# Performance work log

Measured on AMD Instinct MI355X. Metric: run time of the kernel, lower is better.

## Reference

```python
import jax, jax.numpy as jnp
import numpy as np

NUM_C = 1000
B, L = 8, 1024
D, H, NB, DFF = 512, 8, 4, 2048
DK = D // H
EPS = 1e-5


def _ln(x, s, b):
    mu = jnp.mean(x, axis=-1, keepdims=True)
    var = jnp.mean((x - mu) ** 2, axis=-1, keepdims=True)
    return (x - mu) * jax.lax.rsqrt(var + EPS) * s + b


def setup_inputs() -> dict:
    key = jax.random.key(0)
    ks = iter(jax.random.split(key, 64))

    def nrm(shape, scale=0.02):
        return jax.random.normal(next(ks), shape, dtype=jnp.float32) * scale

    inp = {
        "q": jax.random.randint(next(ks), (B, L), 0, NUM_C),
        "r": jax.random.randint(next(ks), (B, L), 0, 2),
        # embeddings
        "ctx_emb": nrm((NUM_C * 2, D)),
        "val_emb": nrm((NUM_C * 2, D)),
        "skill_emb": nrm((NUM_C, D)),
        "pos_emb": nrm((L, D)),
        # attention projections, stacked over blocks
        "Wq": nrm((NB, D, D)), "bq": jnp.zeros((NB, D)),
        "Wk": nrm((NB, D, D)), "bk": jnp.zeros((NB, D)),
        "Wv": nrm((NB, D, D)), "bv": jnp.zeros((NB, D)),
        "Wo": nrm((NB, D, D)), "bo": jnp.zeros((NB, D)),
        # layer norms (ctx / val streams, pre- and post-FFN)
        "ln1c_s": jnp.ones((NB, D)), "ln1c_b": jnp.zeros((NB, D)),
        "ln1v_s": jnp.ones((NB, D)), "ln1v_b": jnp.zeros((NB, D)),
        "ln2c_s": jnp.ones((NB, D)), "ln2c_b": jnp.zeros((NB, D)),
        "ln2v_s": jnp.ones((NB, D)), "ln2v_b": jnp.zeros((NB, D)),
        # FFNs
        "fc1c_W": nrm((NB, D, DFF)), "fc1c_b": jnp.zeros((NB, DFF)),
        "fc2c_W": nrm((NB, DFF, D)), "fc2c_b": jnp.zeros((NB, D)),
        "fc1v_W": nrm((NB, D, DFF)), "fc1v_b": jnp.zeros((NB, DFF)),
        "fc2v_W": nrm((NB, DFF, D)), "fc2v_b": jnp.zeros((NB, D)),
        # prediction head: [3D -> DFF -> 256 -> 1]
        "hW1": nrm((3 * D, DFF)), "hb1": jnp.zeros((DFF,)),
        "hW2": nrm((DFF, 256)), "hb2": jnp.zeros((256,)),
        "hW3": nrm((256, 1)), "hb3": jnp.zeros((1,)),
    }
    return inp


def reference(q, r, ctx_emb, val_emb, skill_emb, pos_emb,
              Wq, bq, Wk, bk, Wv, bv, Wo, bo,
              ln1c_s, ln1c_b, ln1v_s, ln1v_b,
              ln2c_s, ln2c_b, ln2v_s, ln2v_b,
              fc1c_W, fc1c_b, fc2c_W, fc2c_b,
              fc1v_W, fc1v_b, fc2v_W, fc2v_b,
              hW1, hb1, hW2, hb2, hW3, hb3):
    inter = q + NUM_C * r                       # [B, L] interaction ids
    pos = pos_emb[None, :L, :]
    ctx = ctx_emb[inter] + pos                  # [B, L, D]
    val = val_emb[inter] + pos                  # [B, L, D]
    causal = jnp.tril(jnp.ones((L, L), dtype=bool))
    scale = 1.0 / (DK ** 0.5)

    for i in range(NB):
        # dual-stream MHA: Q,K from ctx; V from val
        Q = (ctx @ Wq[i] + bq[i]).reshape(B, L, H, DK)
        K = (ctx @ Wk[i] + bk[i]).reshape(B, L, H, DK)
        V = (val @ Wv[i] + bv[i]).reshape(B, L, H, DK)
        # fp32 scores (as in torch source), mask==0 -> -inf, softmax
        scores = jnp.einsum('bqhd,bkhd->bhqk', Q.astype(jnp.float32),
                            K.astype(jnp.float32)) * scale
        scores = jnp.where(causal, scores, -jnp.inf)
        attn = jax.nn.softmax(scores, axis=-1)  # dropout = identity (eval)
        out = jnp.einsum('bhqk,bkhd->bqhd', attn, V).reshape(B, L, D)
        out = out @ Wo[i] + bo[i]
        # shared attn output added to both streams, separate norms
        ctx = _ln(ctx + out, ln1c_s[i], ln1c_b[i])
        val = _ln(val + out, ln1v_s[i], ln1v_b[i])
        # dual FFNs
        f_ctx = jax.nn.relu(ctx @ fc1c_W[i] + fc1c_b[i]) @ fc2c_W[i] + fc2c_b[i]
        ctx = _ln(ctx + f_ctx, ln2c_s[i], ln2c_b[i])
        f_val = jax.nn.relu(val @ fc1v_W[i] + fc1v_b[i]) @ fc2v_W[i] + fc2v_b[i]
        val = _ln(val + f_val, ln2v_s[i], ln2v_b[i])

    feat = jnp.concatenate([ctx, val, skill_emb[q]], axis=-1)  # [B, L, 3D]
    h = jax.nn.relu(feat @ hW1 + hb1)
    h = jax.nn.relu(h @ hW2 + hb2)
    logits = (h @ hW3 + hb3)[..., 0]
    return jax.nn.sigmoid(logits)               # [B, L] p(correct)
```

## Files before the change

kernel.cpp:

```cpp
#include <hip/hip_runtime.h>
#include <hip/hip_bf16.h>
#include <math.h>

#define TOK 8192
#define DM 512
#define NH 8
#define DKH 64
#define DFFN 2048
#define SEQ 1024
#define NBLK 4
#define NUMC 1000

typedef __attribute__((ext_vector_type(8))) short bf16x8;
typedef __attribute__((ext_vector_type(4))) float f32x4;
typedef __attribute__((ext_vector_type(4))) ushort u16x4;
typedef __hip_bfloat16 bf16;

__device__ __forceinline__ void gload_lds16(const ushort* g, ushort* l) {
    __builtin_amdgcn_global_load_lds(
        (const __attribute__((address_space(1))) void*)g,
        (__attribute__((address_space(3))) void*)l, 16, 0, 0);
}

__device__ __forceinline__ void wgbar() {
    asm volatile("" ::: "memory");
    __builtin_amdgcn_s_barrier();
    asm volatile("" ::: "memory");
}

__global__ __launch_bounds__(256) void embed_kernel(
    const int* __restrict__ q, const int* __restrict__ r,
    const float* __restrict__ ctx_emb, const float* __restrict__ val_emb,
    const float* __restrict__ pos_emb,
    float* __restrict__ ctx32, float* __restrict__ val32,
    bf16* __restrict__ ctx16, bf16* __restrict__ val16)
{
    const int t = blockIdx.x;
    const int inter = q[t] + NUMC * r[t];
    const int l = t & (SEQ - 1);
    const float* ce = ctx_emb + (size_t)inter * DM;
    const float* ve = val_emb + (size_t)inter * DM;
    const float* pe = pos_emb + (size_t)l * DM;
    const size_t o = (size_t)t * DM;
    for (int d = threadIdx.x; d < DM; d += 256) {
        float p = pe[d];
        float c = ce[d] + p;
        float v = ve[d] + p;
        ctx32[o + d] = c; val32[o + d] = v;
        ctx16[o + d] = __float2bfloat16(c);
        val16[o + d] = __float2bfloat16(v);
    }
}

__global__ __launch_bounds__(256) void transpose_kernel(
    const float* __restrict__ src, bf16* __restrict__ dst,
    int K, int N, long sb, long db)
{
    __shared__ float t[32][33];
    src += (long)blockIdx.z * sb;
    dst += (long)blockIdx.z * db;
    const int n0 = blockIdx.x * 32;
    const int k0 = blockIdx.y * 32;
    const int tx = threadIdx.x;
    const int ty = threadIdx.y;
    for (int i = ty; i < 32; i += 8) t[i][tx] = src[(size_t)(k0 + i) * N + n0 + tx];
    __syncthreads();
    for (int i = ty; i < 32; i += 8)
        dst[(size_t)(n0 + i) * K + k0 + tx] = __float2bfloat16(t[tx][i]);
}

template<int BN, bool OUTBF16>
__global__ __launch_bounds__(256, 3) void mfma_gemm(
    const ushort* __restrict__ A, const ushort* __restrict__ Bt,
    const float* __restrict__ bias1, const float* __restrict__ bias2, int split,
    void* __restrict__ Cv, int N, int K, int relu, int vtmode,
    const ushort* __restrict__ A1, const ushort* __restrict__ Bt1,
    const float* __restrict__ bias1_1, void* __restrict__ Cv1)
{
    if (blockIdx.z) { A = A1; Bt = Bt1; bias1 = bias1_1; Cv = Cv1; }
    constexpr int MI = (BN == 128) ? 4 : 2;
    constexpr int BR = BN / 32;
    __shared__ ushort As[128 * 64];
    __shared__ ushort Bs[BN * 64];
    const int tid = threadIdx.x;
    const int wave = tid >> 6;
    const int lane = tid & 63;
    const int ln = lane & 15;
    const int kq = lane >> 4;
    const int nx = gridDim.x;
    const int lin = blockIdx.x + nx * blockIdx.y;
    const int loc = lin >> 3;
    const int mdiv = loc / nx;
    const int bm = ((lin & 7) + 8 * mdiv) * 128;
    const int bn = (loc - mdiv * nx) * BN;
    const int wr = (BN == 128) ? (wave >> 1) * 64 : wave * 32;
    const int wc = (BN == 128) ? (wave & 1) * 64 : 0;

    const int trow = tid >> 3;
    const int gcb = (tid & 7) ^ (trow & 7);
    const ushort* Ab = A + (size_t)(bm + trow) * K + gcb * 8;
    const ushort* Bb = Bt + (size_t)(bn + trow) * K + gcb * 8;
    ushort* AsW = As + wave * 512;
    ushort* BsW = Bs + wave * 512;

    f32x4 acc[MI][4];
#pragma unroll
    for (int i = 0; i < MI; ++i)
#pragma unroll
        for (int j = 0; j < 4; ++j) acc[i][j] = (f32x4){0.f, 0.f, 0.f, 0.f};

    for (int k0 = 0; k0 < K; k0 += 64) {
        __syncthreads();
#pragma unroll
        for (int p = 0; p < 4; ++p)
            gload_lds16(Ab + (size_t)32 * p * K + k0, AsW + p * 2048);
#pragma unroll
        for (int p = 0; p < BR; ++p)
            gload_lds16(Bb + (size_t)32 * p * K + k0, BsW + p * 2048);
        __syncthreads();
#pragma unroll
        for (int half = 0; half < 2; ++half) {
            const int cb = ((half * 4 + kq) ^ (ln & 7)) * 8;
            bf16x8 bfr[4];
#pragma unroll
            for (int j = 0; j < 4; ++j)
                bfr[j] = *(const bf16x8*)&Bs[(wc + j * 16 + ln) * 64 + cb];
#pragma unroll
            for (int i = 0; i < MI; ++i) {
                const bf16x8 af = *(const bf16x8*)&As[(wr + i * 16 + ln) * 64 + cb];
#pragma unroll
                for (int j = 0; j < 4; ++j)
                    acc[i][j] = __builtin_amdgcn_mfma_f32_16x16x32_bf16(af, bfr[j], acc[i][j], 0, 0, 0);
            }
        }
    }

#pragma unroll
    for (int i = 0; i < MI; ++i) {
        const int rowb = bm + wr + i * 16 + kq * 4;
#pragma unroll
        for (int j = 0; j < 4; ++j) {
            const int colg = bn + wc + j * 16 + ln;
            const float bv = (colg < split) ? bias1[colg] : bias2[colg - split];
            if (vtmode) {
                union { u16x4 v; ushort u[4]; } pk;
#pragma unroll
                for (int rr = 0; rr < 4; ++rr) {
                    float v = acc[i][j][rr] + bv;
                    bf16 t = __float2bfloat16(v);
                    pk.u[rr] = *(ushort*)&t;
                }
                *(u16x4*)((ushort*)Cv + ((size_t)(rowb >> 10) * 512 + colg) * 1024 + (rowb & 1023)) = pk.v;
            } else {
#pragma unroll
                for (int rr = 0; rr < 4; ++rr) {
                    float v = acc[i][j][rr] + bv;
                    if (relu) v = fmaxf(v, 0.f);
                    if (OUTBF16)
                        ((bf16*)Cv)[(size_t)(rowb + rr) * N + colg] = __float2bfloat16(v);
                    else
                        ((float*)Cv)[(size_t)(rowb + rr) * N + colg] = v;
                }
            }
        }
    }
}

__device__ __forceinline__ void stage256(const ushort* Ag, const ushort* Bg,
                                         ushort* AsD, ushort* BsD, int K, int kk)
{
#pragma unroll
    for (int p = 0; p < 4; ++p)
        gload_lds16(Ag + (size_t)(64 * p) * K + kk, AsD + p * 4096);
#pragma unroll
    for (int p = 0; p < 4; ++p)
        gload_lds16(Bg + (size_t)(64 * p) * K + kk, BsD + p * 4096);
}

__global__ __launch_bounds__(512, 2) void mfma_gemm256(
    const ushort* __restrict__ A, const ushort* __restrict__ Bt,
    const float* __restrict__ bias, bf16* __restrict__ C, int N, int K, int relu,
    const ushort* __restrict__ A1, const ushort* __restrict__ Bt1,
    const float* __restrict__ bias1, bf16* __restrict__ C1)
{
    if (blockIdx.z) { A = A1; Bt = Bt1; bias = bias1; C = C1; }
    __shared__ ushort As[2 * 16384];
    __shared__ ushort Bs[2 * 16384];
    const int tid = threadIdx.x;
    const int wave = tid >> 6, lane = tid & 63;
    const int ln = lane & 15, kq = lane >> 4;
    const int wr = wave >> 2;
    const int wc = wave & 3;

    const int nx = gridDim.x;
    const int lin = blockIdx.x + nx * blockIdx.y;
    const int loc = lin >> 3;
    const int mdiv = loc / nx;
    const int bm = ((lin & 7) + 8 * mdiv) * 256;
    const int bn = (loc - mdiv * nx) * 256;

    const int srow = tid >> 3;
    const int sgcb = (tid & 7) ^ (srow & 7);
    const ushort* Ag = A + (size_t)(bm + srow) * K + sgcb * 8;
    const ushort* Bg = Bt + (size_t)(bn + srow) * K + sgcb * 8;
    const int wofs = wave * 512;

    f32x4 acc[8][4];
#pragma unroll
    for (int i = 0; i < 8; ++i)
#pragma unroll
        for (int j = 0; j < 4; ++j) acc[i][j] = (f32x4){0.f, 0.f, 0.f, 0.f};

    const int NT = K >> 6;
    stage256(Ag, Bg, As + wofs, Bs + wofs, K, 0);

    for (int t = 0; t < NT; ++t) {
        const int b = t & 1;
        const int k0 = t << 6;
        if (t + 1 < NT) {
            stage256(Ag, Bg, As + (b ^ 1) * 16384 + wofs, Bs + (b ^ 1) * 16384 + wofs, K, k0 + 64);
            asm volatile("s_waitcnt vmcnt(8)" ::: "memory");
        } else {
            asm volatile("s_waitcnt vmcnt(0)" ::: "memory");
        }
        wgbar();

        const ushort* Asb = As + b * 16384;
        const ushort* Bsb = Bs + b * 16384;
        bf16x8 bf[4][2];
#pragma unroll
        for (int j = 0; j < 4; ++j)
#pragma unroll
            for (int h = 0; h < 2; ++h)
                bf[j][h] = *(const bf16x8*)&Bsb[(wc * 64 + j * 16 + ln) * 64 + (((h * 4 + kq) ^ (ln & 7)) * 8)];
#pragma unroll
        for (int q = 0; q < 4; ++q) {
            bf16x8 af0[2], af1[2];
#pragma unroll
            for (int h = 0; h < 2; ++h) {
                af0[h] = *(const bf16x8*)&Asb[(wr * 128 + (2 * q) * 16 + ln) * 64 + (((h * 4 + kq) ^ (ln & 7)) * 8)];
                af1[h] = *(const bf16x8*)&Asb[(wr * 128 + (2 * q + 1) * 16 + ln) * 64 + (((h * 4 + kq) ^ (ln & 7)) * 8)];
            }
            __builtin_amdgcn_s_setprio(1);
#pragma unroll
            for (int h = 0; h < 2; ++h)
#pragma unroll
                for (int j = 0; j < 4; ++j) {
                    acc[2 * q][j]     = __builtin_amdgcn_mfma_f32_16x16x32_bf16(af0[h], bf[j][h], acc[2 * q][j], 0, 0, 0);
                    acc[2 * q + 1][j] = __builtin_amdgcn_mfma_f32_16x16x32_bf16(af1[h], bf[j][h], acc[2 * q + 1][j], 0, 0, 0);
                }
            __builtin_amdgcn_s_setprio(0);
            wgbar();
        }
    }

#pragma unroll
    for (int i = 0; i < 8; ++i) {
        const int gr = bm + wr * 128 + i * 16 + kq * 4;
#pragma unroll
        for (int j = 0; j < 4; ++j) {
            const int gc = bn + wc * 64 + j * 16 + ln;
            const float bv = bias[gc];
#pragma unroll
            for (int rr = 0; rr < 4; ++rr) {
                float v = acc[i][j][rr] + bv;
                if (relu) v = fmaxf(v, 0.f);
                C[(size_t)(gr + rr) * N + gc] = __float2bfloat16(v);
            }
        }
    }
}

__global__ __launch_bounds__(256) void attn_kernel(
    const bf16* __restrict__ QK, const bf16* __restrict__ Vt,
    bf16* __restrict__ Og)
{
    __shared__ ushort Qs[64 * 64];
    __shared__ ushort Ks[64 * 64];
    __shared__ ushort Vs[64 * 64];
    __shared__ ushort Ps[4 * 16 * 68];

    const int tid = threadIdx.x;
    const int wave = tid >> 6, lane = tid & 63;
    const int ln = lane & 15, kq = lane >> 4;
    const int lin = blockIdx.x + 16 * blockIdx.y;
    const int loc = lin >> 3;
    const int qt = loc & 15;
    const int bh = (lin & 7) + 8 * (loc >> 4);
    const int b = bh >> 3, h = bh & 7;

    const int srow = tid >> 3;
    const int sgcb = (tid & 7) ^ (srow & 7);
    const ushort* gQ = (const ushort*)QK + (size_t)(b * SEQ + qt * 64 + srow) * 1024 + h * 64 + sgcb * 8;
    const ushort* gK = (const ushort*)QK + (size_t)(b * SEQ + srow) * 1024 + 512 + h * 64 + sgcb * 8;
    const ushort* gV = (const ushort*)Vt + (size_t)(bh * 64 + srow) * 1024 + sgcb * 8;
    ushort* QsW = Qs + wave * 512;
    ushort* KsW = Ks + wave * 512;
    ushort* VsW = Vs + wave * 512;

    gload_lds16(gQ, QsW);
    gload_lds16(gQ + 32 * 1024, QsW + 2048);

    float rs[4];
    f32x4 oacc[4];
#pragma unroll
    for (int r = 0; r < 4; ++r) { rs[r] = 0.f; oacc[r] = (f32x4){0.f, 0.f, 0.f, 0.f}; }
    const float sc2 = 0.125f * 1.4426950408889634f;

    const int cb0 = (kq ^ (ln & 7)) * 8;
    const int cb1 = ((4 + kq) ^ (ln & 7)) * 8;

    for (int kt = 0; kt <= qt; ++kt) {
        __syncthreads();
        gload_lds16(gK + (size_t)kt * 64 * 1024, KsW);
        gload_lds16(gK + (size_t)(kt * 64 + 32) * 1024, KsW + 2048);
        gload_lds16(gV + kt * 64, VsW);
        gload_lds16(gV + 32 * 1024 + kt * 64, VsW + 2048);
        __syncthreads();

        const bf16x8 aq0 = *(const bf16x8*)&Qs[(wave * 16 + ln) * 64 + cb0];
        const bf16x8 aq1 = *(const bf16x8*)&Qs[(wave * 16 + ln) * 64 + cb1];
        f32x4 s[4];
#pragma unroll
        for (int c = 0; c < 4; ++c) {
            const bf16x8 bk0 = *(const bf16x8*)&Ks[(c * 16 + ln) * 64 + cb0];
            const bf16x8 bk1 = *(const bf16x8*)&Ks[(c * 16 + ln) * 64 + cb1];
            s[c] = (f32x4){0.f, 0.f, 0.f, 0.f};
            s[c] = __builtin_amdgcn_mfma_f32_16x16x32_bf16(aq0, bk0, s[c], 0, 0, 0);
            s[c] = __builtin_amdgcn_mfma_f32_16x16x32_bf16(aq1, bk1, s[c], 0, 0, 0);
        }
        if (kt == qt) {
#pragma unroll
            for (int c = 0; c < 4; ++c)
#pragma unroll
                for (int r = 0; r < 4; ++r) {
                    const int qg = wave * 16 + kq * 4 + r;
                    const int jg = c * 16 + ln;
                    const float pv = (jg <= qg) ? exp2f(s[c][r] * sc2) : 0.f;
                    rs[r] += pv;
                    *(bf16*)&Ps[wave * 1088 + (kq * 4 + r) * 68 + c * 16 + ln] = __float2bfloat16(pv);
                }
        } else {
#pragma unroll
            for (int c = 0; c < 4; ++c)
#pragma unroll
                for (int r = 0; r < 4; ++r) {
                    const float pv = exp2f(s[c][r] * sc2);
                    rs[r] += pv;
                    *(bf16*)&Ps[wave * 1088 + (kq * 4 + r) * 68 + c * 16 + ln] = __float2bfloat16(pv);
                }
        }
        const bf16x8 ap0 = *(const bf16x8*)&Ps[wave * 1088 + ln * 68 + kq * 8];
        const bf16x8 ap1 = *(const bf16x8*)&Ps[wave * 1088 + ln * 68 + 32 + kq * 8];
#pragma unroll
        for (int c2 = 0; c2 < 4; ++c2) {
            const bf16x8 bv0 = *(const bf16x8*)&Vs[(c2 * 16 + ln) * 64 + cb0];
            const bf16x8 bv1 = *(const bf16x8*)&Vs[(c2 * 16 + ln) * 64 + cb1];
            oacc[c2] = __builtin_amdgcn_mfma_f32_16x16x32_bf16(ap0, bv0, oacc[c2], 0, 0, 0);
            oacc[c2] = __builtin_amdgcn_mfma_f32_16x16x32_bf16(ap1, bv1, oacc[c2], 0, 0, 0);
        }
    }
    float inv[4];
#pragma unroll
    for (int r = 0; r < 4; ++r) {
        float v = rs[r];
        v += __shfl_xor(v, 1);
        v += __shfl_xor(v, 2);
        v += __shfl_xor(v, 4);
        v += __shfl_xor(v, 8);
        inv[r] = 1.f / v;
    }
#pragma unroll
    for (int c2 = 0; c2 < 4; ++c2)
#pragma unroll
        for (int r = 0; r < 4; ++r)
            Og[(size_t)(b * SEQ + qt * 64 + wave * 16 + kq * 4 + r) * 512 + h * 64 + c2 * 16 + ln]
                = __float2bfloat16(oacc[c2][r] * inv[r]);
}

__global__ __launch_bounds__(256) void lnp_kernel(
    const float* __restrict__ x0, const bf16* __restrict__ r0, const float* __restrict__ s0,
    const float* __restrict__ b0, float* __restrict__ of0, bf16* __restrict__ oh0,
    const float* __restrict__ x1, const bf16* __restrict__ r1, const float* __restrict__ s1,
    const float* __restrict__ b1, float* __restrict__ of1, bf16* __restrict__ oh1)
{
    const float* x = x0; const bf16* res = r0; const float* s = s0; const float* bb = b0;
    float* of = of0; bf16* oh = oh0;
    if (blockIdx.y) { x = x1; res = r1; s = s1; bb = b1; of = of1; oh = oh1; }
    __shared__ float w1[4], w2[4];
    const size_t o = (size_t)blockIdx.x * DM;
    const int i0 = threadIdx.x, i1 = threadIdx.x + 256;
    const float v0 = x[o + i0] + __bfloat162float(res[o + i0]);
    const float v1 = x[o + i1] + __bfloat162float(res[o + i1]);
    float sum = v0 + v1;
#pragma unroll
    for (int off = 32; off; off >>= 1) sum += __shfl_down(sum, off);
    if ((threadIdx.x & 63) == 0) w1[threadIdx.x >> 6] = sum;
    __syncthreads();
    const float mu = (w1[0] + w1[1] + w1[2] + w1[3]) * (1.f / DM);
    const float d0 = v0 - mu, d1 = v1 - mu;
    float vs = d0 * d0 + d1 * d1;
#pragma unroll
    for (int off = 32; off; off >>= 1) vs += __shfl_down(vs, off);
    if ((threadIdx.x & 63) == 0) w2[threadIdx.x >> 6] = vs;
    __syncthreads();
    const float rstd = rsqrtf((w2[0] + w2[1] + w2[2] + w2[3]) * (1.f / DM) + 1e-5f);
    const float o0 = d0 * rstd * s[i0] + bb[i0];
    const float o1 = d1 * rstd * s[i1] + bb[i1];
    of[o + i0] = o0; of[o + i1] = o1;
    oh[o + i0] = __float2bfloat16(o0);
    oh[o + i1] = __float2bfloat16(o1);
}

__global__ __launch_bounds__(256) void gather_kernel(
    const bf16* __restrict__ ctx16, const bf16* __restrict__ val16,
    const float* __restrict__ skill, const int* __restrict__ q,
    bf16* __restrict__ feat)
{
    const int t = blockIdx.x;
    const float* sp = skill + (size_t)q[t] * DM;
    const bf16* cp = ctx16 + (size_t)t * DM;
    const bf16* vp = val16 + (size_t)t * DM;
    bf16* fp = feat + (size_t)t * (3 * DM);
    for (int d = threadIdx.x; d < DM; d += 256) {
        fp[d] = cp[d];
        fp[DM + d] = vp[d];
        fp[2 * DM + d] = __float2bfloat16(sp[d]);
    }
}

__global__ __launch_bounds__(256) void logits_kernel(
    const float* __restrict__ h2, const float* __restrict__ w,
    const float* __restrict__ bptr, float* __restrict__ out)
{
    __shared__ float w1[4];
    const int t = blockIdx.x;
    float sum = h2[(size_t)t * 256 + threadIdx.x] * w[threadIdx.x];
#pragma unroll
    for (int off = 32; off; off >>= 1) sum += __shfl_down(sum, off);
    if ((threadIdx.x & 63) == 0) w1[threadIdx.x >> 6] = sum;
    __syncthreads();
    if (threadIdx.x == 0) {
        const float logit = w1[0] + w1[1] + w1[2] + w1[3] + bptr[0];
        out[t] = 1.f / (1.f + __expf(-logit));
    }
}

extern "C" void kernel_launch(void* const* d_in, const int* in_sizes, int n_in,
                              void* d_out, int out_size, void* d_ws, size_t ws_size,
                              hipStream_t stream)
{
    const int*   q         = (const int*)d_in[0];
    const int*   r         = (const int*)d_in[1];
    const float* ctx_emb   = (const float*)d_in[2];
    const float* val_emb   = (const float*)d_in[3];
    const float* skill_emb = (const float*)d_in[4];
    const float* pos_emb   = (const float*)d_in[5];
    const float* Wq = (const float*)d_in[6];
    const float* bq = (const float*)d_in[7];
    const float* Wk = (const float*)d_in[8];
    const float* bk = (const float*)d_in[9];
    const float* Wv = (const float*)d_in[10];
    const float* bv = (const float*)d_in[11];
    const float* Wo = (const float*)d_in[12];
    const float* bo = (const float*)d_in[13];
    const float* ln1c_s = (const float*)d_in[14];
    const float* ln1c_b = (const float*)d_in[15];
    const float* ln1v_s = (const float*)d_in[16];
    const float* ln1v_b = (const float*)d_in[17];
    const float* ln2c_s = (const float*)d_in[18];
    const float* ln2c_b = (const float*)d_in[19];
    const float* ln2v_s = (const float*)d_in[20];
    const float* ln2v_b = (const float*)d_in[21];
    const float* fc1c_W = (const float*)d_in[22];
    const float* fc1c_b = (const float*)d_in[23];
    const float* fc2c_W = (const float*)d_in[24];
    const float* fc2c_b = (const float*)d_in[25];
    const float* fc1v_W = (const float*)d_in[26];
    const float* fc1v_b = (const float*)d_in[27];
    const float* fc2v_W = (const float*)d_in[28];
    const float* fc2v_b = (const float*)d_in[29];
    const float* hW1 = (const float*)d_in[30];
    const float* hb1 = (const float*)d_in[31];
    const float* hW2 = (const float*)d_in[32];
    const float* hb2 = (const float*)d_in[33];
    const float* hW3 = (const float*)d_in[34];
    const float* hb3 = (const float*)d_in[35];
    float* out = (float*)d_out;

    char* p = (char*)d_ws;
    auto alloc = [&](size_t bytes) { char* ret = p; p += bytes; return ret; };
    float* ctx32 = (float*)alloc(16777216);
    float* val32 = (float*)alloc(16777216);
    bf16*  ob16c = (bf16*)alloc(8388608);
    bf16*  ob16v = (bf16*)alloc(8388608);
    bf16*  ctx16 = (bf16*)alloc(8388608);
    bf16*  val16 = (bf16*)alloc(8388608);
    bf16*  qk16  = (bf16*)alloc(16777216);
    bf16*  v16pad= (bf16*)alloc(8388608);
    bf16*  vt16  = (bf16*)alloc(8388608);
    bf16*  att16 = (bf16*)alloc(8388608);
    bf16*  mid16c = (bf16*)alloc(33554432);
    bf16*  qkT   = (bf16*)alloc(4194304);
    bf16*  vT    = (bf16*)alloc(2097152);
    bf16*  oT    = (bf16*)alloc(2097152);
    bf16*  fc1cT = (bf16*)alloc(8388608);
    bf16*  fc2cT = (bf16*)alloc(8388608);
    bf16*  fc1vT = (bf16*)alloc(8388608);
    bf16*  fc2vT = (bf16*)alloc(8388608);
    bf16*  hW1T  = (bf16*)alloc(6291456);
    bf16*  hW2T  = (bf16*)alloc(1048576);
    (void)v16pad;
    bf16*  mid16v = qk16;
    bf16*  feat16 = qk16;
    float* h2     = (float*)vt16;

    const dim3 tb(32, 8);
    transpose_kernel<<<dim3(16, 16, 4), tb, 0, stream>>>(Wq, qkT,          512, 512, 262144, 524288);
    transpose_kernel<<<dim3(16, 16, 4), tb, 0, stream>>>(Wk, qkT + 262144, 512, 512, 262144, 524288);
    transpose_kernel<<<dim3(16, 16, 4), tb, 0, stream>>>(Wv, vT, 512, 512, 262144, 262144);
    transpose_kernel<<<dim3(16, 16, 4), tb, 0, stream>>>(Wo, oT, 512, 512, 262144, 262144);
    transpose_kernel<<<dim3(64, 16, 4), tb, 0, stream>>>(fc1c_W, fc1cT, 512, 2048, 1048576, 1048576);
    transpose_kernel<<<dim3(16, 64, 4), tb, 0, stream>>>(fc2c_W, fc2cT, 2048, 512, 1048576, 1048576);
    transpose_kernel<<<dim3(64, 16, 4), tb, 0, stream>>>(fc1v_W, fc1vT, 512, 2048, 1048576, 1048576);
    transpose_kernel<<<dim3(16, 64, 4), tb, 0, stream>>>(fc2v_W, fc2vT, 2048, 512, 1048576, 1048576);
    transpose_kernel<<<dim3(64, 48, 1), tb, 0, stream>>>(hW1, hW1T, 1536, 2048, 0, 0);
    transpose_kernel<<<dim3(8, 64, 1),  tb, 0, stream>>>(hW2, hW2T, 2048, 256, 0, 0);

    embed_kernel<<<TOK, 256, 0, stream>>>(q, r, ctx_emb, val_emb, pos_emb,
                                          ctx32, val32, ctx16, val16);

    for (int i = 0; i < NBLK; ++i) {
        mfma_gemm<128, true><<<dim3(8, 64), 256, 0, stream>>>(
            (const ushort*)ctx16, (const ushort*)(qkT + (size_t)i * 524288),
            bq + i * DM, bk + i * DM, 512, qk16, 1024, 512, 0, 0,
            nullptr, nullptr, nullptr, nullptr);
        mfma_gemm<64, true><<<dim3(8, 64), 256, 0, stream>>>(
            (const ushort*)val16, (const ushort*)(vT + (size_t)i * 262144),
            bv + i * DM, nullptr, 1 << 30, vt16, 512, 512, 0, 1,
            nullptr, nullptr, nullptr, nullptr);
        attn_kernel<<<dim3(16, 64), 256, 0, stream>>>(qk16, vt16, att16);
        mfma_gemm<64, true><<<dim3(8, 64), 256, 0, stream>>>(
            (const ushort*)att16, (const ushort*)(oT + (size_t)i * 262144),
            bo + i * DM, nullptr, 1 << 30, ob16c, 512, 512, 0, 0,
            nullptr, nullptr, nullptr, nullptr);
        lnp_kernel<<<dim3(TOK, 2), 256, 0, stream>>>(
            ctx32, ob16c, ln1c_s + i * DM, ln1c_b + i * DM, ctx32, ctx16,
            val32, ob16c, ln1v_s + i * DM, ln1v_b + i * DM, val32, val16);
        mfma_gemm256<<<dim3(8, 32, 2), 512, 0, stream>>>(
            (const ushort*)ctx16, (const ushort*)(fc1cT + (size_t)i * 1048576),
            fc1c_b + i * DFFN, mid16c, 2048, 512, 1,
            (const ushort*)val16, (const ushort*)(fc1vT + (size_t)i * 1048576),
            fc1v_b + i * DFFN, mid16v);
        mfma_gemm<128, true><<<dim3(4, 64, 2), 256, 0, stream>>>(
            (const ushort*)mid16c, (const ushort*)(fc2cT + (size_t)i * 1048576),
            fc2c_b + i * DM, nullptr, 1 << 30, ob16c, 512, 2048, 0, 0,
            (const ushort*)mid16v, (const ushort*)(fc2vT + (size_t)i * 1048576),
            fc2v_b + i * DM, ob16v);
        lnp_kernel<<<dim3(TOK, 2), 256, 0, stream>>>(
            ctx32, ob16c, ln2c_s + i * DM, ln2c_b + i * DM, ctx32, ctx16,
            val32, ob16v, ln2v_s + i * DM, ln2v_b + i * DM, val32, val16);
    }

    gather_kernel<<<TOK, 256, 0, stream>>>(ctx16, val16, skill_emb, q, feat16);
    mfma_gemm256<<<dim3(8, 32), 512, 0, stream>>>(
        (const ushort*)feat16, (const ushort*)hW1T, hb1, mid16c, 2048, 1536, 1,
        nullptr, nullptr, nullptr, nullptr);
    mfma_gemm<64, false><<<dim3(4, 64), 256, 0, stream>>>(
        (const ushort*)mid16c, (const ushort*)hW2T, hb2, nullptr, 1 << 30, h2, 256, 2048, 1, 0,
        nullptr, nullptr, nullptr, nullptr);
    logits_kernel<<<TOK, 256, 0, stream>>>(h2, hW3, hb3, out);
}
```

Baseline: 1.140 ms.

## Interleave next-tile global-to-LDS loads with MFMA phases in 256 GEMM

Restructures the main loop of the 256x256 GEMM kernel so the prefetch of the next K-tile is split into pieces. B rows load first, then A row groups load between the four MFMA phases, with partial vmcnt waits and barriers placed per phase and a peeled final iteration. The aim is to spread memory traffic across the compute and shorten the stall at each tile boundary. It relies on hand-counted vmcnt values and extra barriers, so a miscount could cause a race or add synchronisation overhead.

```diff
diff --git a/kernel.cpp b/kernel.cpp
--- a/kernel.cpp
+++ b/kernel.cpp
@@ -166,17 +166,6 @@
     }
 }
 
-__device__ __forceinline__ void stage256(const ushort* Ag, const ushort* Bg,
-                                         ushort* AsD, ushort* BsD, int K, int kk)
-{
-#pragma unroll
-    for (int p = 0; p < 4; ++p)
-        gload_lds16(Ag + (size_t)(64 * p) * K + kk, AsD + p * 4096);
-#pragma unroll
-    for (int p = 0; p < 4; ++p)
-        gload_lds16(Bg + (size_t)(64 * p) * K + kk, BsD + p * 4096);
-}
-
 __global__ __launch_bounds__(512, 2) void mfma_gemm256(
     const ushort* __restrict__ A, const ushort* __restrict__ Bt,
     const float* __restrict__ bias, bf16* __restrict__ C, int N, int K, int relu,
@@ -205,6 +194,40 @@
     const ushort* Bg = Bt + (size_t)(bn + srow) * K + sgcb * 8;
     const int wofs = wave * 512;
 
+#define STG_A(p, bb, kk) gload_lds16(Ag + (size_t)(64 * (p)) * K + (kk), As + (bb) * 16384 + (p) * 4096 + wofs)
+#define STG_B(p, bb, kk) gload_lds16(Bg + (size_t)(64 * (p)) * K + (kk), Bs + (bb) * 16384 + (p) * 4096 + wofs)
+
+#define PH(q, WAITASM) { \
+    bf16x8 af0[2], af1[2]; \
+    _Pragma("unroll") \
+    for (int h = 0; h < 2; ++h) { \
+        const int cb = (((h * 4 + kq) ^ (ln & 7)) * 8); \
+        af0[h] = *(const bf16x8*)&Asb[(wr * 128 + (2 * (q)) * 16 + ln) * 64 + cb]; \
+        af1[h] = *(const bf16x8*)&Asb[(wr * 128 + (2 * (q) + 1) * 16 + ln) * 64 + cb]; \
+    } \
+    wgbar(); \
+    asm volatile("s_waitcnt lgkmcnt(0)" ::: "memory"); \
+    __builtin_amdgcn_s_setprio(1); \
+    _Pragma("unroll") \
+    for (int h = 0; h < 2; ++h) { \
+        _Pragma("unroll") \
+        for (int j = 0; j < 4; ++j) { \
+            acc[2 * (q)][j]     = __builtin_amdgcn_mfma_f32_16x16x32_bf16(af0[h], bfr[j][h], acc[2 * (q)][j], 0, 0, 0); \
+            acc[2 * (q) + 1][j] = __builtin_amdgcn_mfma_f32_16x16x32_bf16(af1[h], bfr[j][h], acc[2 * (q) + 1][j], 0, 0, 0); \
+        } \
+    } \
+    __builtin_amdgcn_s_setprio(0); \
+    WAITASM; \
+    wgbar(); }
+
+#define RD_BFR() \
+    _Pragma("unroll") \
+    for (int j = 0; j < 4; ++j) { \
+        _Pragma("unroll") \
+        for (int h = 0; h < 2; ++h) \
+            bfr[j][h] = *(const bf16x8*)&Bsb[(wc * 64 + j * 16 + ln) * 64 + (((h * 4 + kq) ^ (ln & 7)) * 8)]; \
+    }
+
     f32x4 acc[8][4];
 #pragma unroll
     for (int i = 0; i < 8; ++i)
@@ -212,47 +235,43 @@
         for (int j = 0; j < 4; ++j) acc[i][j] = (f32x4){0.f, 0.f, 0.f, 0.f};
 
     const int NT = K >> 6;
-    stage256(Ag, Bg, As + wofs, Bs + wofs, K, 0);
-
-    for (int t = 0; t < NT; ++t) {
+
+    STG_B(0, 0, 0); STG_B(1, 0, 0); STG_B(2, 0, 0); STG_B(3, 0, 0);
+    STG_A(0, 0, 0); STG_A(2, 0, 0);
+    STG_A(1, 0, 0); STG_A(3, 0, 0);
+    asm volatile("s_waitcnt vmcnt(2)" ::: "memory");
+    wgbar();
+
+    for (int t = 0; t < NT - 1; ++t) {
         const int b = t & 1;
-        const int k0 = t << 6;
-        if (t + 1 < NT) {
-            stage256(Ag, Bg, As + (b ^ 1) * 16384 + wofs, Bs + (b ^ 1) * 16384 + wofs, K, k0 + 64);
-            asm volatile("s_waitcnt vmcnt(8)" ::: "memory");
-        } else {
-            asm volatile("s_waitcnt vmcnt(0)" ::: "memory");
-        }
-        wgbar();
-
+        const int kn = (t + 1) << 6;
         const ushort* Asb = As + b * 16384;
         const ushort* Bsb = Bs + b * 16384;
-        bf16x8 bf[4][2];
-#pragma unroll
-        for (int j = 0; j < 4; ++j)
-#pragma unroll
-            for (int h = 0; h < 2; ++h)
-                bf[j][h] = *(const bf16x8*)&Bsb[(wc * 64 + j * 16 + ln) * 64 + (((h * 4 + kq) ^ (ln & 7)) * 8)];
-#pragma unroll
-        for (int q = 0; q < 4; ++q) {
-            bf16x8 af0[2], af1[2];
-#pragma unroll
-            for (int h = 0; h < 2; ++h) {
-                af0[h] = *(const bf16x8*)&Asb[(wr * 128 + (2 * q) * 16 + ln) * 64 + (((h * 4 + kq) ^ (ln & 7)) * 8)];
-                af1[h] = *(const bf16x8*)&Asb[(wr * 128 + (2 * q + 1) * 16 + ln) * 64 + (((h * 4 + kq) ^ (ln & 7)) * 8)];
-            }
-            __builtin_amdgcn_s_setprio(1);
-#pragma unroll
-            for (int h = 0; h < 2; ++h)
-#pragma unroll
-                for (int j = 0; j < 4; ++j) {
-                    acc[2 * q][j]     = __builtin_amdgcn_mfma_f32_16x16x32_bf16(af0[h], bf[j][h], acc[2 * q][j], 0, 0, 0);
-                    acc[2 * q + 1][j] = __builtin_amdgcn_mfma_f32_16x16x32_bf16(af1[h], bf[j][h], acc[2 * q + 1][j], 0, 0, 0);
-                }
-            __builtin_amdgcn_s_setprio(0);
-            wgbar();
-        }
-    }
+        bf16x8 bfr[4][2];
+        STG_B(0, b ^ 1, kn); STG_B(1, b ^ 1, kn); STG_B(2, b ^ 1, kn); STG_B(3, b ^ 1, kn);
+        RD_BFR();
+        PH(0, )
+        STG_A(0, b ^ 1, kn); STG_A(2, b ^ 1, kn);
+        PH(1, asm volatile("s_waitcnt vmcnt(6)" ::: "memory"))
+        STG_A(1, b ^ 1, kn); STG_A(3, b ^ 1, kn);
+        PH(2, )
+        PH(3, asm volatile("s_waitcnt vmcnt(2)" ::: "memory"))
+    }
+    {
+        const int b = (NT - 1) & 1;
+        const ushort* Asb = As + b * 16384;
+        const ushort* Bsb = Bs + b * 16384;
+        bf16x8 bfr[4][2];
+        RD_BFR();
+        PH(0, )
+        PH(1, asm volatile("s_waitcnt vmcnt(0)" ::: "memory"))
+        PH(2, )
+        PH(3, )
+    }
+#undef PH
+#undef RD_BFR
+#undef STG_A
+#undef STG_B
 
 #pragma unroll
     for (int i = 0; i < 8; ++i) {
```

New measurement: 1.191 ms. 4.5% more time.
